# Optimization experiments

Measured on AMD Instinct MI355X. Metric: run time of the kernel, lower is better.

Reference implementation:

```python
import jax, jax.numpy as jnp
import numpy as np

EPS = 1e-5
SLOPE = 0.2

def _lrelu(x):
    return jnp.where(x >= 0, x, SLOPE * x)

def _bn(x, axes):
    # BatchNorm in training mode with gamma=1, beta=0 (module defaults), biased var
    m = jnp.mean(x, axis=axes, keepdims=True)
    v = jnp.var(x, axis=axes, keepdims=True)
    return (x - m) * jax.lax.rsqrt(v + EPS)

def _knn(x, k):
    # x: [B, C, N] -> idx [B, N, k] of nearest neighbors (incl. self)
    inner = -2.0 * jnp.einsum('bcn,bcm->bnm', x, x)
    xx = jnp.sum(x * x, axis=1)  # [B, N]
    d = -xx[:, :, None] - inner - xx[:, None, :]  # negative squared dist
    return jax.lax.top_k(d, k)[1]

def _graph_feature(x, k):
    # x: [B, C, N] -> [B, 2C, N, k] of (neighbor - center, center)
    idx = _knn(x, k)                       # [B, N, k]
    xt = jnp.transpose(x, (0, 2, 1))       # [B, N, C]
    feat = jax.vmap(lambda xb, ib: xb[ib])(xt, idx)  # [B, N, k, C]
    center = xt[:, :, None, :]
    out = jnp.concatenate([feat - center, jnp.broadcast_to(center, feat.shape)], axis=-1)
    return jnp.transpose(out, (0, 3, 1, 2))

def _conv2(w, x):   # 1x1 conv2d: x [B,C,N,K]
    return jnp.einsum('oc,bcnk->bonk', w, x)

def _conv1(w, x):   # 1x1 conv1d: x [B,C,N]
    return jnp.einsum('oc,bcn->bon', w, x)

def _pool(xyz, feature, wp, bp, kp):
    # dropout is identity in eval mode
    proj = _conv1(wp, feature) + bp[None, :, None]     # [B, C, N]
    vector = jnp.max(proj, axis=-1, keepdims=True)     # [B, C, 1]
    scores = jax.nn.sigmoid(jnp.sum(feature * vector, axis=1))  # [B, N]
    values, idx = jax.lax.top_k(scores, kp)            # [B, kp]
    node_static = jnp.take_along_axis(xyz, idx[:, None, :], axis=2)
    node_feature = jnp.take_along_axis(feature, idx[:, None, :], axis=2)
    v = values[:, None, :]
    return node_static * v, node_feature * v


def setup_inputs() -> dict:
    key = jax.random.key(0)
    ks = jax.random.split(key, 20)
    def rn(i, shape, s=0.05):
        return jax.random.normal(ks[i], shape, dtype=jnp.float32) * s
    return {
        'x': jax.random.normal(ks[0], (16, 3, 2048), dtype=jnp.float32),
        'w1': rn(1, (64, 6)), 'w2': rn(2, (64, 128)), 'w2m': rn(3, (1024, 128)),
        'w3': rn(4, (128, 256)), 'w4': rn(5, (128, 256)), 'w4m': rn(6, (1024, 256)),
        'w5': rn(7, (256, 512)), 'w5m': rn(8, (1024, 256)),
        'wp1': rn(9, (128, 128)), 'bp1': rn(10, (128,)),
        'wp2': rn(11, (256, 256)), 'bp2': rn(12, (256,)),
        'wl1': rn(13, (512, 3072)),
        'wl2': rn(14, (256, 512)), 'bl2': rn(15, (256,)),
        'wl3': rn(16, (40, 256)), 'bl3': rn(17, (40,)),
    }


def reference(x, w1, w2, w2m, w3, w4, w4m, w5, w5m, wp1, bp1, wp2, bp2, wl1, wl2, bl2, wl3, bl3):
    k = 20
    xyz = x
    # stage 1 (N=2048)
    h = _lrelu(_bn(_conv2(w1, _graph_feature(x, k)), (0, 2, 3)))
    x1 = jnp.max(h, axis=-1)                       # [B, 64, N]
    h = _lrelu(_bn(_conv2(w2, _graph_feature(x1, k)), (0, 2, 3)))
    x2 = jnp.max(h, axis=-1)                       # [B, 64, N]
    xt1_ = jnp.concatenate([x1, x2], axis=1)       # [B, 128, N]
    xt1 = _lrelu(_bn(_conv1(w2m, xt1_), (0, 2)))   # [B, 1024, N]
    node1, nf1 = _pool(xyz, xt1_, wp1, bp1, 256)   # [B,3,256], [B,128,256]
    # stage 2 (256 nodes, k//2)
    h = _lrelu(_bn(_conv2(w3, _graph_feature(nf1, k // 2)), (0, 2, 3)))
    x3 = jnp.max(h, axis=-1)                       # [B, 128, 256]
    h = _lrelu(_bn(_conv2(w4, _graph_feature(x3, k // 2)), (0, 2, 3)))
    x4 = jnp.max(h, axis=-1)
    xt2_ = jnp.concatenate([x3, x4], axis=1)       # [B, 256, 256]
    xt2 = _lrelu(_bn(_conv1(w4m, xt2_), (0, 2)))   # [B, 1024, 256]
    node2, nf2 = _pool(node1, xt2_, wp2, bp2, 64)  # [B,3,64], [B,256,64]
    # stage 3 (64 nodes, k//4)
    h = _lrelu(_bn(_conv2(w5, _graph_feature(nf2, k // 4)), (0, 2, 3)))
    x5 = jnp.max(h, axis=-1)                       # [B, 256, 64]
    xt3 = _lrelu(_bn(_conv1(w5m, x5), (0, 2)))     # [B, 1024, 64]
    # global max pools + head (dropout = identity in eval)
    g = jnp.concatenate([jnp.max(xt1, -1), jnp.max(xt2, -1), jnp.max(xt3, -1)], axis=1)  # [B, 3072]
    h = _lrelu(_bn(g @ wl1.T, (0,)))
    h = _lrelu(_bn(h @ wl2.T + bl2, (0,)))
    out = h @ wl3.T + bl3                          # [B, 40]
    return (out, node1, node2)
```

## Files before the change

### kernel.cpp

```cpp
#include <hip/hip_runtime.h>
#include <cmath>
#include <cstdint>
#include <cstddef>

typedef unsigned int u32;
typedef unsigned short u16;
typedef unsigned long long u64;
typedef __attribute__((ext_vector_type(8))) short short8v;
typedef __attribute__((ext_vector_type(4))) float f32x4;

#define TPB 256
#define EPSV 1e-5f
#define SLP 0.2f

__device__ __forceinline__ float lrelu(float x){ return x >= 0.f ? x : SLP*x; }
__device__ __forceinline__ u32 encf(float f){ u32 u=__float_as_uint(f); return (u&0x80000000u)? ~u : (u|0x80000000u); }
__device__ __forceinline__ float decf(u32 e){ return (e&0x80000000u)? __uint_as_float(e&0x7FFFFFFFu) : __uint_as_float(~e); }
__device__ __forceinline__ u16 f2b(float f){ u32 u=__float_as_uint(f); return (u16)((u + 0x7FFFu + ((u>>16)&1u))>>16); }
__device__ __forceinline__ float b2f(u16 h){ return __uint_as_float(((u32)h)<<16); }

__global__ void k_detect(const u16* __restrict__ raw, int n, int* __restrict__ flag){
  __shared__ float red[TPB];
  int tid=threadIdx.x; float m=0.f;
  for(int i=tid;i<n;i+=TPB){
    float v=fabsf(b2f(raw[i]));
    if(!isnan(v) && !isinf(v) && v>m) m=v;
  }
  red[tid]=m; __syncthreads();
  for(int s=TPB/2;s>0;s>>=1){ if(tid<s) red[tid]=fmaxf(red[tid],red[tid+s]); __syncthreads(); }
  if(tid==0) *flag = (red[0] > 1000.f) ? 1 : 0;
}

struct CvtArgs{ const void* s[18]; float* d[18]; int n[18]; };
__global__ void k_cvt_all(CvtArgs a, const int* __restrict__ flag){
  int z=blockIdx.y; int n=a.n[z]; int f=*flag;
  const void* s=a.s[z]; float* d=a.d[z];
  for(int i=blockIdx.x*TPB+threadIdx.x; i<n; i+=gridDim.x*TPB)
    d[i] = f ? ((const float*)s)[i] : b2f(((const u16*)s)[i]);
}

__global__ void k_castw(const float* __restrict__ W, u16* __restrict__ Wb, int n){
  int i=blockIdx.x*TPB+threadIdx.x; if(i<n) Wb[i]=f2b(W[i]);
}

__global__ void k_xpose_bf(const float* __restrict__ X, u16* __restrict__ Xb,
                           int ldC, int C, int N){
  __shared__ float t[32][33];
  int b=blockIdx.z;
  int c0=blockIdx.y*32, n0=blockIdx.x*32;
  int tx=threadIdx.x&31, ty=threadIdx.x>>5;
  const float* Xs = X + (size_t)b*ldC*N;
  #pragma unroll
  for(int i=0;i<4;i++){
    int c=c0+ty+i*8;
    t[ty+i*8][tx] = (c<C && n0+tx<N) ? Xs[(size_t)c*N + n0+tx] : 0.f;
  }
  __syncthreads();
  u16* Ob = Xb + (size_t)b*N*C;
  #pragma unroll
  for(int i=0;i<4;i++){
    int n=n0+ty+i*8;
    if(n<N && c0+tx<C) Ob[(size_t)n*C + c0+tx] = f2b(t[tx][ty+i*8]);
  }
}

template<int KSTEPS>
__global__ __launch_bounds__(256) void k_convmax_mfma(
    const u16* __restrict__ Wb, const u16* __restrict__ Xb,
    u32* __restrict__ gmaxEnc, int gstride, int g_off, double* __restrict__ stats,
    int C, int N, int O){
  int tid=threadIdx.x, lane=tid&63, w=tid>>6;
  int b=blockIdx.z;
  int oW = blockIdx.y*64 + w*16;
  int nB = blockIdx.x*256;
  int row16 = lane&15, grp = lane>>4;
  short8v af[KSTEPS];
  const u16* Wrow = Wb + (size_t)(oW + row16)*C + grp*8;
  #pragma unroll
  for(int ks=0;ks<KSTEPS;ks++) af[ks] = *(const short8v*)(Wrow + ks*32);
  const short8v zb = {0,0,0,0,0,0,0,0};
  f32x4 acc[16];
  #pragma unroll
  for(int t=0;t<16;t++){
    int n = nB + t*16 + row16;
    bool nv = (n < N);
    const u16* Xrow = Xb + ((size_t)b*N + (nv? n:0))*C + grp*8;
    short8v bf[KSTEPS];
    #pragma unroll
    for(int ks=0;ks<KSTEPS;ks++) bf[ks] = nv ? *(const short8v*)(Xrow + ks*32) : zb;
    f32x4 a = {0.f,0.f,0.f,0.f};
    #pragma unroll
    for(int ks=0;ks<KSTEPS;ks++)
      a = __builtin_amdgcn_mfma_f32_16x16x32_bf16(af[ks], bf[ks], a, 0, 0, 0);
    acc[t]=a;
  }
  float mxr[4], s1r[4], s2r[4];
  #pragma unroll
  for(int r=0;r<4;r++){ mxr[r]=-INFINITY; s1r[r]=0.f; s2r[r]=0.f; }
  #pragma unroll
  for(int t=0;t<16;t++){
    int n = nB + t*16 + row16;
    bool nv = (n<N);
    #pragma unroll
    for(int r=0;r<4;r++){
      float y = acc[t][r];
      if(nv){ mxr[r]=fmaxf(mxr[r],y); s1r[r]+=y; s2r[r]+=y*y; }
    }
  }
  #pragma unroll
  for(int s=1;s<16;s<<=1){
    #pragma unroll
    for(int r=0;r<4;r++){
      mxr[r]=fmaxf(mxr[r], __shfl_xor(mxr[r], s));
      s1r[r]+=__shfl_xor(s1r[r], s);
      s2r[r]+=__shfl_xor(s2r[r], s);
    }
  }
  if(row16==0){
    #pragma unroll
    for(int r=0;r<4;r++){
      int o = oW + grp*4 + r;
      atomicMax(&gmaxEnc[(size_t)b*gstride + g_off + o], encf(mxr[r]));
      atomicAdd(&stats[2*o], (double)s1r[r]);
      atomicAdd(&stats[2*o+1], (double)s2r[r]);
    }
  }
}

__global__ void k_sqnorm(const float* __restrict__ X, float* __restrict__ xx, int B, int ldC, int C, int N){
  int i=blockIdx.x*TPB+threadIdx.x; if(i>=B*N) return;
  int b=i/N, n=i-b*N;
  const float* p = X + ((size_t)b*ldC)*N + n;
  float s=0.f;
  for(int c=0;c<C;c++){ float x=p[(size_t)c*N]; s+=x*x; }
  xx[i]=s;
}

template<int CT>
__global__ __launch_bounds__(256, 6) void k_knn2048(
    const float* __restrict__ X, const float* __restrict__ xx,
    int ldC, int KSEL, int* __restrict__ idxOut){
  const int N = 2048;
  extern __shared__ float sm[];
  __shared__ u64 cand[4][128];
  int tid=threadIdx.x, lane=tid&63, w=tid>>6;
  int b=blockIdx.y, row0=blockIdx.x*4;
  const float* Xb = X + (size_t)b*ldC*N;
  const float* xxb = xx + (size_t)b*N;
  int c0 = tid*4;
  u32 ev[32];

  #pragma unroll
  for(int h=0;h<2;h++){
    float4 acc[4];
    #pragma unroll
    for(int r=0;r<4;r++) acc[r]=make_float4(0.f,0.f,0.f,0.f);
    #pragma unroll 2
    for(int c=0;c<CT;c++){
      const float* Xc = Xb + (size_t)c*N;
      float4 bv = *(const float4*)(Xc + h*1024 + c0);
      #pragma unroll
      for(int r=0;r<4;r++){
        float a = Xc[row0+r];
        acc[r].x += a*bv.x; acc[r].y += a*bv.y;
        acc[r].z += a*bv.z; acc[r].w += a*bv.w;
      }
    }
    float4 xm = *(const float4*)&xxb[h*1024 + c0];
    #pragma unroll
    for(int r=0;r<4;r++){
      float xr = xxb[row0+r];
      float4 d;
      d.x=2.f*acc[r].x-xr-xm.x; d.y=2.f*acc[r].y-xr-xm.y;
      d.z=2.f*acc[r].z-xr-xm.z; d.w=2.f*acc[r].w-xr-xm.w;
      *(float4*)&sm[r*1024 + c0] = d;
    }
    __syncthreads();
    const float* Sr = sm + (size_t)w*1024;
    #pragma unroll
    for(int ch=0;ch<4;ch++){
      float4 v = *(const float4*)&Sr[ch*256 + lane*4];
      int base = h*16 + ch*4;
      ev[base+0]=encf(v.x); ev[base+1]=encf(v.y);
      ev[base+2]=encf(v.z); ev[base+3]=encf(v.w);
    }
    if(h==0) __syncthreads();
  }

  u64* cw = cand[w];
  int* op = idxOut + ((size_t)b*N + row0 + w)*KSEL;
  u32 vmax=ev[0];
  #pragma unroll
  for(int j=1;j<32;j++) vmax = vmax>ev[j]? vmax:ev[j];
  u32 lo=0u, hi=0xFFFFFFFFu;
  while(lo<hi){
    u32 d=hi-lo; u32 mid=lo+(d>>1)+(d&1u);
    int cnum=(int)__popcll(__ballot(vmax>=mid));
    if(cnum>=KSEL) lo=mid; else hi=mid-1u;
  }
  u32 T=lo;
  u64 lml=((u64)1<<lane)-1ull;
  u32 base=0;
  #pragma unroll
  for(int j=0;j<32;j++){
    bool p = ev[j]>=T;
    u64 mk=__ballot(p);
    u32 pos=base+(u32)__popcll(mk&lml);
    int m = (j>>2)*256 + lane*4 + (j&3);
    if(p && pos<128u) cw[pos] = ((u64)ev[j]<<32) | (u64)(u32)(~(u32)m);
    base += (u32)__popcll(mk);
  }
  int nc=(int)base;
  if(nc<=64){
    u64 cv = cw[lane];
    if(lane>=nc) cv=0ull;
    #pragma unroll
    for(int kk=2;kk<=64;kk<<=1){
      #pragma unroll
      for(int jj=kk>>1;jj>0;jj>>=1){
        u64 p=__shfl_xor(cv,jj);
        bool takeMax=(((lane&jj)!=0)==((lane&kk)==0));
        u64 mx=cv>p?cv:p, mn=cv>p?p:cv;
        cv=takeMax?mx:mn;
      }
    }
    if(lane>=64-KSEL) op[63-lane]=(int)(~(u32)cv);
  } else if(nc<=128){
    u64 c0v=cw[lane], c1v=cw[64+lane];
    if(64+lane>=nc) c1v=0ull;
    u64 kl=~0ull;
    for(int t=0;t<KSEL;t++){
      u64 bk=(c0v<kl)?c0v:0ull;
      if(c1v<kl&&c1v>bk) bk=c1v;
      #pragma unroll
      for(int s=1;s<64;s<<=1){u64 ok=__shfl_xor(bk,s); if(ok>bk)bk=ok;}
      if(lane==0) op[t]=(int)(~(u32)bk);
      kl=bk;
    }
  } else {
    u64 kl=~0ull;
    for(int t=0;t<KSEL;t++){
      u64 bk=0ull;
      #pragma unroll
      for(int j=0;j<32;j++){
        int m = (j>>2)*256 + lane*4 + (j&3);
        u64 kj=((u64)ev[j]<<32)|(u64)(u32)(~(u32)m);
        if(kj<kl&&kj>bk) bk=kj;
      }
      #pragma unroll
      for(int s=1;s<64;s<<=1){u64 ok=__shfl_xor(bk,s); if(ok>bk)bk=ok;}
      if(lane==0) op[t]=(int)(~(u32)bk);
      kl=bk;
    }
  }
}

template<int JMAX, int CT>
__global__ __launch_bounds__(256) void k_knn_fused(
    const float* __restrict__ X, const float* __restrict__ xx,
    int ldC, int KSEL, int* __restrict__ idxOut){
  const int N = JMAX*64;
  extern __shared__ float sm[];
  __shared__ u64 cand[4][128];
  int tid=threadIdx.x, lane=tid&63, w=tid>>6;
  int b=blockIdx.y, row0=blockIdx.x*4;
  const float* Xb = X + (size_t)b*ldC*N;
  const float* xxb = xx + (size_t)b*N;

  {
    int tcol = (tid < N)? tid : (tid & (N-1));
    float acc[4];
    #pragma unroll
    for(int r=0;r<4;r++) acc[r]=0.f;
    #pragma unroll 4
    for(int c=0;c<CT;c++){
      const float* Xc = Xb + (size_t)c*N;
      float bv = Xc[tcol];
      #pragma unroll
      for(int r=0;r<4;r++) acc[r] += Xc[row0+r]*bv;
    }
    float xm = xxb[tcol];
    #pragma unroll
    for(int r=0;r<4;r++) sm[r*N + tcol] = 2.f*acc[r] - xxb[row0+r] - xm;
  }
  __syncthreads();

  u64* cw = cand[w];
  int r = w;
  const float* Sr = sm + (size_t)r*N;
  u32 ev[JMAX];
  if constexpr (JMAX>=4){
    #pragma unroll
    for(int ch=0;ch<JMAX/4;ch++){
      float4 v = *(const float4*)&Sr[ch*256 + lane*4];
      ev[ch*4+0]=encf(v.x); ev[ch*4+1]=encf(v.y); ev[ch*4+2]=encf(v.z); ev[ch*4+3]=encf(v.w);
    }
  } else {
    ev[0]=encf(Sr[lane]);
  }
  int* op = idxOut + ((size_t)b*N + row0 + r)*KSEL;
  if constexpr (JMAX>=8){
    u32 vmax=ev[0];
    #pragma unroll
    for(int j=1;j<JMAX;j++) vmax = vmax>ev[j]? vmax:ev[j];
    u32 lo=0u, hi=0xFFFFFFFFu;
    while(lo<hi){
      u32 d=hi-lo; u32 mid=lo+(d>>1)+(d&1u);
      int cnum=(int)__popcll(__ballot(vmax>=mid));
      if(cnum>=KSEL) lo=mid; else hi=mid-1u;
    }
    u32 T=lo;
    u64 lml=((u64)1<<lane)-1ull;
    u32 base=0;
    #pragma unroll
    for(int j=0;j<JMAX;j++){
      bool p = ev[j]>=T;
      u64 mk=__ballot(p);
      u32 pos=base+(u32)__popcll(mk&lml);
      int m = (j>>2)*256 + lane*4 + (j&3);
      if(p && pos<128u) cw[pos] = ((u64)ev[j]<<32) | (u64)(u32)(~(u32)m);
      base += (u32)__popcll(mk);
    }
    int nc=(int)base;
    if(nc<=64){
      u64 cv = cw[lane];
      if(lane>=nc) cv=0ull;
      #pragma unroll
      for(int kk=2;kk<=64;kk<<=1){
        #pragma unroll
        for(int jj=kk>>1;jj>0;jj>>=1){
          u64 p=__shfl_xor(cv,jj);
          bool takeMax=(((lane&jj)!=0)==((lane&kk)==0));
          u64 mx=cv>p?cv:p, mn=cv>p?p:cv;
          cv=takeMax?mx:mn;
        }
      }
      if(lane>=64-KSEL) op[63-lane]=(int)(~(u32)cv);
    } else if(nc<=128){
      u64 c0v=cw[lane], c1v=cw[64+lane];
      if(64+lane>=nc) c1v=0ull;
      u64 kl=~0ull;
      for(int t=0;t<KSEL;t++){
        u64 bk=(c0v<kl)?c0v:0ull;
        if(c1v<kl&&c1v>bk) bk=c1v;
        #pragma unroll
        for(int s=1;s<64;s<<=1){u64 ok=__shfl_xor(bk,s); if(ok>bk)bk=ok;}
        if(lane==0) op[t]=(int)(~(u32)bk);
        kl=bk;
      }
    } else {
      u64 kl=~0ull;
      for(int t=0;t<KSEL;t++){
        u64 bk=0ull;
        #pragma unroll
        for(int j=0;j<JMAX;j++){
          int m = (j>>2)*256 + lane*4 + (j&3);
          u64 kj=((u64)ev[j]<<32)|(u64)(u32)(~(u32)m);
          if(kj<kl&&kj>bk) bk=kj;
        }
        #pragma unroll
        for(int s=1;s<64;s<<=1){u64 ok=__shfl_xor(bk,s); if(ok>bk)bk=ok;}
        if(lane==0) op[t]=(int)(~(u32)bk);
        kl=bk;
      }
    }
  } else {
    u64 key[JMAX];
    #pragma unroll
    for(int j=0;j<JMAX;j++){
      int m = (JMAX>=4)? ((j>>2)*256 + lane*4 + (j&3)) : lane;
      key[j]=((u64)ev[j]<<32)|(u64)(u32)(~(u32)m);
    }
    u64 kl=~0ull;
    for(int t=0;t<KSEL;t++){
      u64 bk=0ull;
      #pragma unroll
      for(int j=0;j<JMAX;j++){ u64 kj=key[j]; if(kj<kl&&kj>bk) bk=kj; }
      #pragma unroll
      for(int s=1;s<64;s<<=1){u64 ok=__shfl_xor(bk,s); if(ok>bk)bk=ok;}
      if(lane==0) op[t]=(int)(~(u32)bk);
      kl=bk;
    }
  }
}

__global__ void k_topk_sort(const float* __restrict__ S, int M, int K,
                            int* __restrict__ idxOut, float* __restrict__ valOut){
  extern __shared__ u64 key[];
  int b=blockIdx.x, tid=threadIdx.x;
  const float* Sr = S + (size_t)b*M;
  for(int i=tid;i<M;i+=TPB)
    key[i] = ((u64)(~encf(Sr[i]))<<32) | (u32)i;
  __syncthreads();
  for(int k=2;k<=M;k<<=1){
    for(int j=k>>1;j>0;j>>=1){
      for(int i=tid;i<M;i+=TPB){
        int ixj=i^j;
        if(ixj>i){
          u64 a=key[i], c=key[ixj];
          bool up=((i&k)==0);
          if(up ? (a>c) : (a<c)){ key[i]=c; key[ixj]=a; }
        }
      }
      __syncthreads();
    }
  }
  for(int p=tid;p<K;p+=TPB){
    u64 kk=key[p];
    idxOut[(size_t)b*K+p]=(int)(u32)(kk&0xFFFFFFFFull);
    valOut[(size_t)b*K+p]=decf(~(u32)(kk>>32));
  }
}

__global__ void k_uv(const float* __restrict__ X, int ldC, const float* __restrict__ W,
                     float* __restrict__ U, float* __restrict__ V, int C, int N, int O){
  int n=blockIdx.x*TPB+threadIdx.x; if(n>=N) return;
  int o=blockIdx.y, b=blockIdx.z;
  const float* Xb = X + ((size_t)b*ldC)*N + n;
  const float* Wr = W + (size_t)o*2*C;
  float u=0,v=0;
  for(int c=0;c<C;c++){ float x=Xb[(size_t)c*N]; float wa=Wr[c], wb=Wr[C+c]; u+=wa*x; v+=(wb-wa)*x; }
  size_t off=((size_t)b*O+o)*N+n; U[off]=u; V[off]=v;
}

template<int KT, int OT>
__global__ void k_nbr_t(const float* __restrict__ U, const float* __restrict__ V, const int* __restrict__ idx,
                        float* __restrict__ outBase, int ldCout, int ch_off,
                        double* __restrict__ stats, int O, int N){
  __shared__ double redS[4][OT], redQ[4][OT];
  int tid=threadIdx.x, lane=tid&63, wv=tid>>6;
  int n = blockIdx.x*TPB+tid;
  int o0 = blockIdx.y*OT, b = blockIdx.z;
  bool act = (n<N);
  int nc = act? n : (N-1);
  int jr[KT];
  const int* jp = idx + ((size_t)b*N+nc)*KT;
  #pragma unroll
  for(int k=0;k<KT;k++){ int j=jp[k]; jr[k] = ((unsigned)j<(unsigned)N)? j : 0; }
  for(int oo=0;oo<OT;oo++){
    const float* Ur = U + ((size_t)b*O+o0+oo)*N;
    float mx=-INFINITY, s1=0.f, s2=0.f;
    #pragma unroll
    for(int k=0;k<KT;k++){ float u=Ur[jr[k]]; mx=fmaxf(mx,u); s1+=u; s2+=u*u; }
    float v = V[((size_t)b*O+o0+oo)*N+nc];
    if(act) outBase[((size_t)b*ldCout+ch_off+o0+oo)*N+n] = mx+v;
    double cs = act ? ((double)s1 + (double)KT*(double)v) : 0.0;
    double cq = act ? ((double)s2 + 2.0*(double)v*(double)s1 + (double)KT*(double)v*(double)v) : 0.0;
    #pragma unroll
    for(int s=1;s<64;s<<=1){ cs += __shfl_xor(cs,s); cq += __shfl_xor(cq,s); }
    if(lane==0){ redS[wv][oo]=cs; redQ[wv][oo]=cq; }
  }
  __syncthreads();
  if(tid<OT){
    double s=0,q=0;
    #pragma unroll
    for(int w=0;w<4;w++){ s+=redS[w][tid]; q+=redQ[w][tid]; }
    atomicAdd(&stats[2*(o0+tid)], s);
    atomicAdd(&stats[2*(o0+tid)+1], q);
  }
}

__global__ void k_bnact(float* __restrict__ out, int ldCout, int ch_off, const double* __restrict__ stats,
                        int O, int N, double cnt){
  int n=blockIdx.x*TPB+threadIdx.x; if(n>=N) return;
  int o=blockIdx.y, b=blockIdx.z;
  double m=stats[2*o]/cnt;
  double var=stats[2*o+1]/cnt - m*m;
  float s=rsqrtf((float)var+EPSV);
  size_t p=((size_t)b*ldCout+ch_off+o)*N+n;
  float h=out[p];
  out[p] = lrelu((float)((double)h-m)*s);
}

template<int PTS>
__global__ void k_convmax(const float* __restrict__ X, int ldC, const float* __restrict__ W, const float* __restrict__ bias,
                          u32* __restrict__ gmaxEnc, int gstride, int g_off, double* __restrict__ stats,
                          int C, int N, int O){
  __shared__ float red[4*16*3];
  int tid=threadIdx.x, ot=blockIdx.y, b=blockIdx.z;
  int lane=tid&63, wv=tid>>6;
  int n0 = blockIdx.x*TPB*PTS + tid*PTS;
  bool act = (n0 < N);
  int n0c = act ? n0 : (N-PTS);
  const float* Xb = X + ((size_t)b*ldC)*N;
  const float* Wr = W + (size_t)ot*16*C;
  float acc[16][PTS];
  #pragma unroll
  for(int oo=0;oo<16;oo++)
    #pragma unroll
    for(int p=0;p<PTS;p++) acc[oo][p]=0.f;
  for(int c=0;c<C;c+=4){
    float xv[4][PTS];
    #pragma unroll
    for(int cc=0;cc<4;cc++){
      if(PTS==4){
        float4 t = *(const float4*)&Xb[(size_t)(c+cc)*N + n0c];
        xv[cc][0]=t.x; xv[cc][1]=t.y; xv[cc][2]=t.z; xv[cc][3]=t.w;
      } else {
        xv[cc][0]=Xb[(size_t)(c+cc)*N + n0c];
      }
    }
    #pragma unroll
    for(int oo=0;oo<16;oo++){
      float w0=Wr[oo*C+c], w1=Wr[oo*C+c+1], w2=Wr[oo*C+c+2], w3=Wr[oo*C+c+3];
      #pragma unroll
      for(int p=0;p<PTS;p++)
        acc[oo][p] += w0*xv[0][p] + w1*xv[1][p] + w2*xv[2][p] + w3*xv[3][p];
    }
  }
  bool hs = (stats!=nullptr);
  #pragma unroll
  for(int oo=0;oo<16;oo++){
    float bval = bias? bias[ot*16+oo] : 0.f;
    float mx=-INFINITY, s1=0.f, s2=0.f;
    #pragma unroll
    for(int p=0;p<PTS;p++){
      float y=acc[oo][p]+bval;
      if(act && n0+p<N){ mx=fmaxf(mx,y); s1+=y; s2+=y*y; }
    }
    #pragma unroll
    for(int s=1;s<64;s<<=1){
      mx=fmaxf(mx,__shfl_xor(mx,s));
      if(hs){ s1+=__shfl_xor(s1,s); s2+=__shfl_xor(s2,s); }
    }
    if(lane==0){ red[(wv*16+oo)*3]=mx; red[(wv*16+oo)*3+1]=s1; red[(wv*16+oo)*3+2]=s2; }
  }
  __syncthreads();
  if(tid<16){
    int oo=tid, o=ot*16+oo;
    float mx=red[oo*3], s1=red[oo*3+1], s2=red[oo*3+2];
    #pragma unroll
    for(int w=1;w<4;w++){ mx=fmaxf(mx,red[(w*16+oo)*3]); s1+=red[(w*16+oo)*3+1]; s2+=red[(w*16+oo)*3+2]; }
    atomicMax(&gmaxEnc[(size_t)b*gstride+g_off+o], encf(mx));
    if(hs){ atomicAdd(&stats[2*o],(double)s1); atomicAdd(&stats[2*o+1],(double)s2); }
  }
}

__global__ void k_gfinal(const u32* __restrict__ gmaxEnc, int gstride, int g_off, const double* __restrict__ stats,
                         float* __restrict__ G, int B, int O, double cnt){
  int i=blockIdx.x*TPB+threadIdx.x; if(i>=B*O) return;
  int b=i/O, o=i-b*O;
  double m=stats[2*o]/cnt;
  double var=stats[2*o+1]/cnt - m*m;
  float s=rsqrtf((float)var+EPSV);
  float x=decf(gmaxEnc[(size_t)b*gstride+g_off+o]);
  G[(size_t)b*gstride+g_off+o]=lrelu((float)((double)x-m)*s);
}

__global__ void k_scores(const float* __restrict__ X, int ldC, const u32* __restrict__ vecEnc,
                         float* __restrict__ sc, int C, int N){
  int n=blockIdx.x*TPB+threadIdx.x; if(n>=N) return;
  int b=blockIdx.y;
  const float* Xb = X + ((size_t)b*ldC)*N + n;
  double s=0;
  for(int c=0;c<C;c++) s += (double)Xb[(size_t)c*N]*(double)decf(vecEnc[(size_t)b*C+c]);
  float sf=(float)s;
  sc[(size_t)b*N+n]=1.f/(1.f+expf(-sf));
}

__global__ void k_pgather(const float* __restrict__ xyz, int ldCx, const float* __restrict__ feat, int ldCf,
                          const int* __restrict__ pidx, const float* __restrict__ pval,
                          float* __restrict__ nodeOut, float* __restrict__ nfOut, int Cf, int Nin, int Kp){
  int b=blockIdx.y;
  int i=blockIdx.x*TPB+threadIdx.x;
  int total=(3+Cf)*Kp; if(i>=total) return;
  int c=i/Kp, p=i-c*Kp;
  int j=pidx[(size_t)b*Kp+p]; if((unsigned)j>=(unsigned)Nin) j=0;
  float v=pval[(size_t)b*Kp+p];
  if(c<3) nodeOut[((size_t)b*3+c)*Kp+p]=xyz[((size_t)b*ldCx+c)*Nin+j]*v;
  else { int cf=c-3; nfOut[((size_t)b*Cf+cf)*Kp+p]=feat[((size_t)b*ldCf+cf)*Nin+j]*v; }
}

__global__ void k_fc_wave(const float* __restrict__ A, const float* __restrict__ W, const float* __restrict__ bias,
                          float* __restrict__ Y, int B, int IN, int OUT){
  int gw = (blockIdx.x*blockDim.x + threadIdx.x) >> 6;
  if(gw >= B*OUT) return;
  int lane = threadIdx.x & 63;
  int b = gw/OUT, j = gw - b*OUT;
  const float4* a4 = (const float4*)(A + (size_t)b*IN);
  const float4* w4 = (const float4*)(W + (size_t)j*IN);
  int n4 = IN >> 2;
  float s = 0.f;
  for(int t=lane; t<n4; t+=64){
    float4 av=a4[t], wv=w4[t];
    s += av.x*wv.x + av.y*wv.y + av.z*wv.z + av.w*wv.w;
  }
  #pragma unroll
  for(int sh=1; sh<64; sh<<=1) s += __shfl_xor(s, sh);
  if(lane==0) Y[gw] = s + (bias? bias[j]:0.f);
}

__global__ void k_bnb(const float* __restrict__ Y, float* __restrict__ H, int B, int F){
  int f=blockIdx.x*TPB+threadIdx.x; if(f>=F) return;
  double s=0,q=0;
  for(int b=0;b<B;b++){ double y=Y[(size_t)b*F+f]; s+=y; q+=y*y; }
  double m=s/B, var=q/B-m*m;
  float sc=rsqrtf((float)var+EPSV);
  for(int b=0;b<B;b++){ float y=Y[(size_t)b*F+f]; H[(size_t)b*F+f]=lrelu((float)((double)y-m)*sc); }
}

__global__ void k_out(const float* __restrict__ OUTF, const float* __restrict__ N1v, const float* __restrict__ N2v,
                      void* __restrict__ dout, const int* __restrict__ flag){
  int i=blockIdx.x*TPB+threadIdx.x; if(i>=16000) return;
  float v = (i<640)? OUTF[i] : (i<12928)? N1v[i-640] : N2v[i-12928];
  if(*flag) ((float*)dout)[i]=v; else ((u16*)dout)[i]=f2b(v);
}

extern "C" void kernel_launch(void* const* d_in, const int* in_sizes, int n_in,
                              void* d_out, int out_size, void* d_ws, size_t ws_size,
                              hipStream_t stream){
  const int B=16;
  char* basep=(char*)d_ws; size_t off=0;
  auto alloc=[&](size_t elems, size_t esz)->void*{
    off=(off+255)&~(size_t)255; void* p=basep+off; off+=elems*esz; return p;
  };
  const int NINP=18;
  const int insz[NINP]={98304,384,8192,131072,32768,32768,262144,131072,262144,16384,128,65536,256,1572864,131072,256,10240,40};
  float* F[NINP];
  for(int i=0;i<NINP;i++) F[i]=(float*)alloc((size_t)insz[i],4);
  float* XF=F[0];
  float *W1F=F[1],*W2F=F[2],*W2MF=F[3],*W3F=F[4],*W4F=F[5],*W4MF=F[6],*W5F=F[7],*W5MF=F[8],
        *WP1F=F[9],*BP1F=F[10],*WP2F=F[11],*BP2F=F[12],*WL1F=F[13],*WL2F=F[14],*BL2F=F[15],*WL3F=F[16],*BL3F=F[17];
  float* XX  =(float*)alloc((size_t)16*2048,4);
  float* U   =(float*)alloc((size_t)16*64*2048,4);
  float* V   =(float*)alloc((size_t)16*64*2048,4);
  float* XT1 =(float*)alloc((size_t)16*128*2048,4);
  float* XT2 =(float*)alloc((size_t)16*256*256,4);
  float* NF1 =(float*)alloc((size_t)16*128*256,4);
  float* NF2 =(float*)alloc((size_t)16*256*64,4);
  float* X5  =(float*)alloc((size_t)16*256*64,4);
  float* NODE1=(float*)alloc((size_t)16*3*256,4);
  float* NODE2=(float*)alloc((size_t)16*3*64,4);
  float* SCORES=(float*)alloc((size_t)16*2048,4);
  float* PVAL1=(float*)alloc((size_t)16*256,4);
  float* PVAL2=(float*)alloc((size_t)16*64,4);
  float* G   =(float*)alloc((size_t)16*3072,4);
  float* Y1  =(float*)alloc((size_t)16*512,4);
  float* H1  =(float*)alloc((size_t)16*512,4);
  float* Y2  =(float*)alloc((size_t)16*256,4);
  float* H2  =(float*)alloc((size_t)16*256,4);
  float* OUTF=(float*)alloc((size_t)16*40,4);
  u32* GMAX  =(u32*)alloc((size_t)16*3072,4);
  u32* VECENC=(u32*)alloc((size_t)16*256,4);
  int* IDX   =(int*)alloc((size_t)16*2048*20,4);
  int* PIDX1 =(int*)alloc((size_t)16*256,4);
  int* PIDX2 =(int*)alloc((size_t)16*64,4);
  double* STATS=(double*)alloc((size_t)2*1024,8);
  int* FLAG  =(int*)alloc(64,4);
  u16* XTB  =(u16*)alloc((size_t)16*2048*128,2);
  u16* WB2M =(u16*)alloc((size_t)131072,2);
  u16* WB4M =(u16*)alloc((size_t)262144,2);
  u16* WB5M =(u16*)alloc((size_t)262144,2);

  k_detect<<<dim3(1),dim3(TPB),0,stream>>>((const u16*)d_in[1], insz[1], FLAG);
  CvtArgs ca;
  for(int i=0;i<NINP;i++){ ca.s[i]=d_in[i]; ca.d[i]=F[i]; ca.n[i]=insz[i]; }
  k_cvt_all<<<dim3(64,NINP),dim3(TPB),0,stream>>>(ca, FLAG);
  k_castw<<<dim3((131072+TPB-1)/TPB),dim3(TPB),0,stream>>>(W2MF,WB2M,131072);
  k_castw<<<dim3((262144+TPB-1)/TPB),dim3(TPB),0,stream>>>(W4MF,WB4M,262144);
  k_castw<<<dim3((262144+TPB-1)/TPB),dim3(TPB),0,stream>>>(W5MF,WB5M,262144);

  auto knn=[&](const float* X, int ldC, int C, int N, int K){
    k_sqnorm<<<dim3((B*N+TPB-1)/TPB),dim3(TPB),0,stream>>>(X,XX,B,ldC,C,N);
    if(N==2048 && C==3)       k_knn2048<3>  <<<dim3(N/4,B),dim3(256),16384,stream>>>(X,XX,ldC,K,IDX);
    else if(N==2048)          k_knn2048<64> <<<dim3(N/4,B),dim3(256),16384,stream>>>(X,XX,ldC,K,IDX);
    else if(N==256){
      size_t shm=(size_t)4*N*4;
      k_knn_fused<4,128> <<<dim3(N/4,B),dim3(256),shm,stream>>>(X,XX,ldC,K,IDX);
    } else {
      size_t shm=(size_t)4*N*4;
      k_knn_fused<1,256> <<<dim3(N/4,B),dim3(256),shm,stream>>>(X,XX,ldC,K,IDX);
    }
  };

  auto graph_conv=[&](const float* X, int ldC, int C, int N, int K, const float* W, int O,
                      float* outBase, int ldCout, int ch_off){
    knn(X,ldC,C,N,K);
    k_uv<<<dim3((N+TPB-1)/TPB,O,B),dim3(TPB),0,stream>>>(X,ldC,W,U,V,C,N,O);
    hipMemsetAsync(STATS,0,2*(size_t)O*sizeof(double),stream);
    dim3 g((N+TPB-1)/TPB, O/8, B);
    if(K==20)      k_nbr_t<20,8><<<g,dim3(TPB),0,stream>>>(U,V,IDX,outBase,ldCout,ch_off,STATS,O,N);
    else if(K==10) k_nbr_t<10,8><<<g,dim3(TPB),0,stream>>>(U,V,IDX,outBase,ldCout,ch_off,STATS,O,N);
    else           k_nbr_t<5,8> <<<g,dim3(TPB),0,stream>>>(U,V,IDX,outBase,ldCout,ch_off,STATS,O,N);
    double cnt=(double)B*(double)N*(double)K;
    k_bnact<<<dim3((N+TPB-1)/TPB,O,B),dim3(TPB),0,stream>>>(outBase,ldCout,ch_off,STATS,O,N,cnt);
  };

  auto convmax_f32=[&](const float* X,int ldC,const float* W,const float* bias,
                   u32* gmax,int gstride,int g_off,double* stats,int C,int N,int O){
    if(N>=1024) k_convmax<4><<<dim3((N+TPB*4-1)/(TPB*4),O/16,B),dim3(TPB),0,stream>>>(X,ldC,W,bias,gmax,gstride,g_off,stats,C,N,O);
    else        k_convmax<1><<<dim3((N+TPB-1)/TPB,O/16,B),dim3(TPB),0,stream>>>(X,ldC,W,bias,gmax,gstride,g_off,stats,C,N,O);
  };

  auto pool=[&](const float* xyzF,int ldCx,const float* featF,int ldCf,int Cf,int Nin,
                const float* WP,const float* BP,int Op,int Kp,
                float* nodeOut,float* nfOut,int* pidx,float* pval){
    hipMemsetAsync(VECENC,0,(size_t)B*Op*4,stream);
    convmax_f32(featF,ldCf,WP,BP,VECENC,Op,0,(double*)nullptr,Cf,Nin,Op);
    k_scores<<<dim3((Nin+TPB-1)/TPB,B),dim3(TPB),0,stream>>>(featF,ldCf,VECENC,SCORES,Cf,Nin);
    k_topk_sort<<<dim3(B),dim3(TPB),(size_t)Nin*8,stream>>>(SCORES,Nin,Kp,pidx,pval);
    k_pgather<<<dim3(((3+Cf)*Kp+TPB-1)/TPB,B),dim3(TPB),0,stream>>>(xyzF,ldCx,featF,ldCf,pidx,pval,nodeOut,nfOut,Cf,Nin,Kp);
  };

  auto gseg=[&](const float* X,int ldC,int C,int N,const u16* WBc,int g_off,double cnt){
    hipMemsetAsync(STATS,0,2*1024*sizeof(double),stream);
    k_xpose_bf<<<dim3((N+31)/32,(C+31)/32,B),dim3(256),0,stream>>>(X,XTB,ldC,C,N);
    dim3 g((N+255)/256, 1024/64, B);
    if(C==128) k_convmax_mfma<4><<<g,dim3(256),0,stream>>>(WBc,XTB,GMAX,3072,g_off,STATS,C,N,1024);
    else       k_convmax_mfma<8><<<g,dim3(256),0,stream>>>(WBc,XTB,GMAX,3072,g_off,STATS,C,N,1024);
    k_gfinal<<<dim3((B*1024+TPB-1)/TPB),dim3(TPB),0,stream>>>(GMAX,3072,g_off,STATS,G,B,1024,cnt);
  };

  graph_conv(XF,3,3,2048,20,W1F,64,XT1,128,0);
  graph_conv(XT1,128,64,2048,20,W2F,64,XT1,128,64);
  hipMemsetAsync(GMAX,0,(size_t)16*3072*4,stream);
  gseg(XT1,128,128,2048,WB2M,0,(double)16*2048);
  pool(XF,3,XT1,128,128,2048,WP1F,BP1F,128,256,NODE1,NF1,PIDX1,PVAL1);
  graph_conv(NF1,128,128,256,10,W3F,128,XT2,256,0);
  graph_conv(XT2,256,128,256,10,W4F,128,XT2,256,128);
  gseg(XT2,256,256,256,WB4M,1024,(double)16*256);
  pool(NODE1,3,XT2,256,256,256,WP2F,BP2F,256,64,NODE2,NF2,PIDX2,PVAL2);
  graph_conv(NF2,256,256,64,5,W5F,256,X5,256,0);
  gseg(X5,256,256,64,WB5M,2048,(double)16*64);
  k_fc_wave<<<dim3((16*512*64+TPB-1)/TPB),dim3(TPB),0,stream>>>(G,WL1F,(const float*)nullptr,Y1,16,3072,512);
  k_bnb<<<dim3((512+TPB-1)/TPB),dim3(TPB),0,stream>>>(Y1,H1,16,512);
  k_fc_wave<<<dim3((16*256*64+TPB-1)/TPB),dim3(TPB),0,stream>>>(H1,WL2F,BL2F,Y2,16,512,256);
  k_bnb<<<dim3((256+TPB-1)/TPB),dim3(TPB),0,stream>>>(Y2,H2,16,256);
  k_fc_wave<<<dim3((16*40*64+TPB-1)/TPB),dim3(TPB),0,stream>>>(H2,WL3F,BL3F,OUTF,16,256,40);
  k_out<<<dim3((16000+TPB-1)/TPB),dim3(TPB),0,stream>>>(OUTF,NODE1,NODE2,(u16*)d_out,FLAG);
}
```

Before: 1.193 ms.

## Widen knn2048 blocks to 8 rows and 512 threads with shared row cache

The 2048-point kNN kernel now processes 8 query rows per block with 512 threads (8 wavefronts) instead of 4 rows with 256 threads. Each column tile loaded from global memory is reused across 8 rows, and the query-row coordinates and squared norms are staged once in shared memory rather than re-read from global in the inner loop. This cuts redundant global loads of the distance operands, in exchange for doubled dynamic shared memory, larger blocks and higher register pressure under launch_bounds(512,6), which may lower occupancy.

```diff
diff --git a/kernel.cpp b/kernel.cpp
--- a/kernel.cpp
+++ b/kernel.cpp
@@ -137,43 +137,53 @@
 }
 
 template<int CT>
-__global__ __launch_bounds__(256, 6) void k_knn2048(
+__global__ __launch_bounds__(512, 6) void k_knn2048(
     const float* __restrict__ X, const float* __restrict__ xx,
     int ldC, int KSEL, int* __restrict__ idxOut){
   const int N = 2048;
   extern __shared__ float sm[];
-  __shared__ u64 cand[4][128];
+  __shared__ u64 cand[8][128];
+  __shared__ float rowA[CT][8];
+  __shared__ float rowXX[8];
   int tid=threadIdx.x, lane=tid&63, w=tid>>6;
-  int b=blockIdx.y, row0=blockIdx.x*4;
+  int b=blockIdx.y, row0=blockIdx.x*8;
   const float* Xb = X + (size_t)b*ldC*N;
   const float* xxb = xx + (size_t)b*N;
-  int c0 = tid*4;
+
+  if(tid < CT*8){ int c=tid>>3, r=tid&7; rowA[c][r]=Xb[(size_t)c*N + row0 + r]; }
+  if(tid < 8) rowXX[tid]=xxb[row0+tid];
+  __syncthreads();
+
+  int c0 = tid*2;
   u32 ev[32];
-
   #pragma unroll
   for(int h=0;h<2;h++){
-    float4 acc[4];
-    #pragma unroll
-    for(int r=0;r<4;r++) acc[r]=make_float4(0.f,0.f,0.f,0.f);
+    float2 acc[8];
+    #pragma unroll
+    for(int r=0;r<8;r++) acc[r]=make_float2(0.f,0.f);
     #pragma unroll 2
     for(int c=0;c<CT;c++){
       const float* Xc = Xb + (size_t)c*N;
-      float4 bv = *(const float4*)(Xc + h*1024 + c0);
-      #pragma unroll
-      for(int r=0;r<4;r++){
-        float a = Xc[row0+r];
-        acc[r].x += a*bv.x; acc[r].y += a*bv.y;
-        acc[r].z += a*bv.z; acc[r].w += a*bv.w;
-      }
-    }
-    float4 xm = *(const float4*)&xxb[h*1024 + c0];
-    #pragma unroll
-    for(int r=0;r<4;r++){
-      float xr = xxb[row0+r];
-      float4 d;
-      d.x=2.f*acc[r].x-xr-xm.x; d.y=2.f*acc[r].y-xr-xm.y;
-      d.z=2.f*acc[r].z-xr-xm.z; d.w=2.f*acc[r].w-xr-xm.w;
-      *(float4*)&sm[r*1024 + c0] = d;
+      float2 bv = *(const float2*)(Xc + h*1024 + c0);
+      float4 alo = *(const float4*)&rowA[c][0];
+      float4 ahi = *(const float4*)&rowA[c][4];
+      acc[0].x += alo.x*bv.x; acc[0].y += alo.x*bv.y;
+      acc[1].x += alo.y*bv.x; acc[1].y += alo.y*bv.y;
+      acc[2].x += alo.z*bv.x; acc[2].y += alo.z*bv.y;
+      acc[3].x += alo.w*bv.x; acc[3].y += alo.w*bv.y;
+      acc[4].x += ahi.x*bv.x; acc[4].y += ahi.x*bv.y;
+      acc[5].x += ahi.y*bv.x; acc[5].y += ahi.y*bv.y;
+      acc[6].x += ahi.z*bv.x; acc[6].y += ahi.z*bv.y;
+      acc[7].x += ahi.w*bv.x; acc[7].y += ahi.w*bv.y;
+    }
+    float2 xm = *(const float2*)&xxb[h*1024 + c0];
+    #pragma unroll
+    for(int r=0;r<8;r++){
+      float xr = rowXX[r];
+      float2 d;
+      d.x=2.f*acc[r].x - xr - xm.x;
+      d.y=2.f*acc[r].y - xr - xm.y;
+      *(float2*)&sm[r*1024 + c0] = d;
     }
     __syncthreads();
     const float* Sr = sm + (size_t)w*1024;
@@ -662,8 +672,8 @@
 
   auto knn=[&](const float* X, int ldC, int C, int N, int K){
     k_sqnorm<<<dim3((B*N+TPB-1)/TPB),dim3(TPB),0,stream>>>(X,XX,B,ldC,C,N);
-    if(N==2048 && C==3)       k_knn2048<3>  <<<dim3(N/4,B),dim3(256),16384,stream>>>(X,XX,ldC,K,IDX);
-    else if(N==2048)          k_knn2048<64> <<<dim3(N/4,B),dim3(256),16384,stream>>>(X,XX,ldC,K,IDX);
+    if(N==2048 && C==3)       k_knn2048<3>  <<<dim3(N/8,B),dim3(512),32768,stream>>>(X,XX,ldC,K,IDX);
+    else if(N==2048)          k_knn2048<64> <<<dim3(N/8,B),dim3(512),32768,stream>>>(X,XX,ldC,K,IDX);
     else if(N==256){
       size_t shm=(size_t)4*N*4;
       k_knn_fused<4,128> <<<dim3(N/4,B),dim3(256),shm,stream>>>(X,XX,ldC,K,IDX);
```

New measurement: 1.225 ms. 1.03x slower.
